# Kernel tuning notes

Hardware: AMD Instinct MI355X
Metric: run time of the kernel (lower is better)

The kernel has to match this reference:

```python
import jax, jax.numpy as jnp
import numpy as np

MUL = 16            # multiplicity of 0e and 1o irreps (in and out)
N_NODES = 10000
N_EDGES = 160000
EDGE_FDIM = 128
H_DIM = 128
WNUM = 4 * MUL * MUL  # 4 instructions x (16 u x 1 v x 16 w) = 1024 weights per edge


def setup_inputs() -> dict:
    key = jax.random.key(0)
    ks = jax.random.split(key, 6)
    x = jax.random.normal(ks[0], (N_NODES, 4 * MUL), dtype=jnp.float32)  # 16x0e + 16x1o -> dim 64
    edge_index = jax.random.randint(ks[1], (2, N_EDGES), 0, N_NODES, dtype=jnp.int32)
    edge_attr = jax.random.normal(ks[2], (N_EDGES, EDGE_FDIM), dtype=jnp.float32)
    edge_sh = jax.random.normal(ks[3], (N_EDGES, 4), dtype=jnp.float32)  # 1x0e + 1x1o
    fc_w1 = jax.random.normal(ks[4], (EDGE_FDIM, H_DIM), dtype=jnp.float32) / np.sqrt(EDGE_FDIM)
    fc_b1 = jnp.zeros((H_DIM,), jnp.float32)
    fc_w2 = jax.random.normal(ks[5], (H_DIM, WNUM), dtype=jnp.float32) / np.sqrt(H_DIM)
    fc_b2 = jnp.zeros((WNUM,), jnp.float32)
    return dict(x=x, edge_index=edge_index, edge_attr=edge_attr, edge_sh=edge_sh,
                fc_w1=fc_w1, fc_b1=fc_b1, fc_w2=fc_w2, fc_b2=fc_b2)


def _tensor_product(xe, edge_sh, w):
    """FullyConnectedTensorProduct('16x0e+16x1o', '1x0e+1x1o', '16x0e+16x1o'),
    shared_weights=False. Instructions (uvw, v=1):
      0e x 0e -> 0e ; 0e x 1o -> 1o ; 1o x 0e -> 1o ; 1o x 1o -> 0e (dot / sqrt(3)).
    Path alpha = 1/sqrt(fan_in) with fan_in = 2*MUL per output irrep (2 paths x 16x1)."""
    x0 = xe[:, :MUL]                          # [E, 16] scalars
    x1 = xe[:, MUL:].reshape(-1, MUL, 3)      # [E, 16, 3] vectors
    sh0 = edge_sh[:, 0:1]                     # [E, 1]
    sh1 = edge_sh[:, 1:4]                     # [E, 3]
    wp = w.reshape(-1, 4, MUL, MUL)           # [E, 4 paths, u, w]
    w00, w01, w10, w11 = wp[:, 0], wp[:, 1], wp[:, 2], wp[:, 3]
    alpha = 1.0 / np.sqrt(2.0 * MUL)
    dot = jnp.einsum('eum,em->eu', x1, sh1)   # 1o . 1o -> 0e
    out0 = alpha * (jnp.einsum('eu,euw->ew', x0 * sh0, w00)
                    + jnp.einsum('eu,euw->ew', dot, w11) / np.sqrt(3.0))  # [E, 16]
    out1 = alpha * (jnp.einsum('eu,euw,em->ewm', x0, w01, sh1)
                    + jnp.einsum('eum,euw->ewm', x1 * sh0[:, :, None], w10))  # [E, 16, 3]
    return jnp.concatenate([out0, out1.reshape(-1, 3 * MUL)], axis=-1)  # [E, 64]


def reference(x, edge_index, edge_attr, edge_sh, fc_w1, fc_b1, fc_w2, fc_b2):
    src, dst = edge_index[0], edge_index[1]
    # per-edge tensor-product weights from edge features (dropout p=0 -> identity)
    w = jax.nn.relu(edge_attr @ fc_w1 + fc_b1) @ fc_w2 + fc_b2       # [E, 1024]
    tp_out = _tensor_product(x[src], edge_sh, w)                      # gather + TP
    seg = jax.ops.segment_sum(tp_out, dst, num_segments=N_NODES)      # scatter-add
    cnt = jax.ops.segment_sum(jnp.ones((N_EDGES,), tp_out.dtype), dst, num_segments=N_NODES)
    out = seg / jnp.maximum(cnt, 1.0)[:, None]                        # mean aggregation
    # residual: out_dim == in_dim (64), so F.pad is a no-op
    return out + x
```

## Files before the change

### kernel.cpp

```cpp
#include <hip/hip_runtime.h>
#include <stdint.h>

#define E_TOTAL 160000
#define NODES   10000
#define FDIM    128
#define HDIM    128
#define WN      1024
#define CDIM    64
#define EPB     32
#define NTHR    256

typedef __bf16 bf16x8 __attribute__((ext_vector_type(8)));
typedef __bf16 bf16x4 __attribute__((ext_vector_type(4)));
typedef float  f32x4  __attribute__((ext_vector_type(4)));

#define MFMA16(a,b,c) __builtin_amdgcn_mfma_f32_16x16x32_bf16(a,b,c,0,0,0)

#define WS_W1B (512*1024)
#define WS_CNT (576*1024)

__device__ __forceinline__ f32x4 ntload4(const float* p) {
    return __builtin_nontemporal_load((const f32x4*)p);
}

__global__ void prep_kernel(const float* __restrict__ W1, const float* __restrict__ W2,
                            __bf16* __restrict__ W1B, __bf16* __restrict__ W2B,
                            float* __restrict__ out_acc, int* __restrict__ cnt) {
    const int b   = blockIdx.x;
    const int tid = threadIdx.x;
    if (b < 72) {
        const float* W = (b < 64) ? W2 : W1;
        __bf16* outB   = (b < 64) ? W2B : W1B;
        const int N    = (b < 64) ? WN : HDIM;
        const int tile = (b < 64) ? b : (b - 64);
        const int lane = tid & 63, ks = tid >> 6;
        const int n  = tile * 16 + (lane & 15);
        const int k0 = ks * 32 + (lane >> 4) * 8;
        bf16x8 hi;
        #pragma unroll
        for (int j = 0; j < 8; ++j) hi[j] = (__bf16)W[(size_t)(k0 + j) * N + n];
        *(bf16x8*)(outB + ((size_t)(tile * 4 + ks) * 64 + lane) * 8) = hi;
    } else {
        const int zt     = (b - 72) * NTHR + tid;
        const int stride = ((int)gridDim.x - 72) * NTHR;
        const float4 z4 = make_float4(0.f, 0.f, 0.f, 0.f);
        for (int i = zt; i < NODES * CDIM / 4; i += stride) ((float4*)out_acc)[i] = z4;
        for (int i = zt; i < NODES; i += stride) cnt[i] = 0;
    }
}

#define ZS 68
__global__ __launch_bounds__(NTHR, 4)
void fused_edge_kernel(const float* __restrict__ x,
                       const int*   __restrict__ edge_index,
                       const float* __restrict__ edge_attr,
                       const float* __restrict__ edge_sh,
                       const float* __restrict__ fc_b1,
                       const float* __restrict__ fc_b2,
                       const __bf16* __restrict__ W1B,
                       const __bf16* __restrict__ W2B,
                       float* __restrict__ out_acc,
                       int*   __restrict__ cnt)
{
    __shared__ __align__(16) char s_arena[25152];
    __bf16* s_attr = (__bf16*)s_arena;
    __bf16* s_h    = (__bf16*)s_arena;
    float (*s_f)[16][32] = (float (*)[16][32])(s_arena + 8192);
    float*  s_b2s  = (float*)(s_arena + 20480);
    float (*s_sh1)[36] = (float (*)[36])(s_arena + 24576);
    int*    s_dst  = (int*)(s_arena + 25024);

    const int tid  = threadIdx.x;
    const int w    = tid >> 6;
    const int th   = w >> 1;
    const int kh   = w & 1;
    const int lane = tid & 63;
    const int quad = lane >> 4;
    const int li   = lane & 15;
    const int e0   = blockIdx.x * EPB;

    if (lane < 32) {
        const int e  = lane;
        const int up = w * 4;
        const int ge = e0 + e;
        const int src = edge_index[ge];
        const f32x4 sh4 = ntload4(edge_sh + (size_t)ge * 4);
        if (tid < EPB) {
            const int d = edge_index[E_TOTAL + ge];
            s_dst[e] = d;
            atomicAdd(&cnt[d], 1);
            s_sh1[0][e] = sh4.y; s_sh1[1][e] = sh4.z; s_sh1[2][e] = sh4.w;
        }
        const float* xp = x + (size_t)src * CDIM;
        const float4 x0v = *(const float4*)(xp + up);
        const float4 xa  = *(const float4*)(xp + 16 + up * 3);
        const float4 xb  = *(const float4*)(xp + 16 + up * 3 + 4);
        const float4 xc  = *(const float4*)(xp + 16 + up * 3 + 8);
        const float x1v[4][3] = {
            {xa.x, xa.y, xa.z}, {xa.w, xb.x, xb.y},
            {xb.z, xb.w, xc.x}, {xc.y, xc.z, xc.w}};
        const float x0a[4] = {x0v.x, x0v.y, x0v.z, x0v.w};
        const float alpha = 0.17677669529663689f;
        const float ai3   = alpha * 0.57735026918962576f;
        const float sh0 = sh4.x;
        #pragma unroll
        for (int j = 0; j < 4; ++j) {
            const int u = up + j;
            const float x0u = x0a[j];
            s_f[0][u][e] = alpha * sh0 * x0u;
            s_f[1][u][e] = alpha * x0u;
            s_f[2][u][e] = alpha * sh0 * x1v[j][0];
            s_f[3][u][e] = alpha * sh0 * x1v[j][1];
            s_f[4][u][e] = alpha * sh0 * x1v[j][2];
            s_f[5][u][e] = ai3 * (x1v[j][0]*sh4.y + x1v[j][1]*sh4.z + x1v[j][2]*sh4.w);
        }
    }
    #pragma unroll
    for (int t4 = 0; t4 < 4; ++t4) {
        const int t = tid + t4 * NTHR;
        const int e = t >> 5, i4 = t & 31;
        const f32x4 v = ntload4(edge_attr + (size_t)(e0 + e) * FDIM + i4 * 4);
        const int f = i4 >> 3, j0 = (i4 & 1) * 4, qc = (i4 >> 1) & 3;
        const int g = e >> 4, lc = e & 15;
        bf16x4 bv = {(__bf16)v[0], (__bf16)v[1], (__bf16)v[2], (__bf16)v[3]};
        *(bf16x4*)(s_attr + (((f * 2 + g) * 64 + qc * 16 + lc) * 8 + j0)) = bv;
    }
    *(f32x4*)&s_b2s[tid * 4] = *(const f32x4*)(fc_b2 + tid * 4);
    __syncthreads();

    {
        const int nt0 = w * 2;
        const float b1a = fc_b1[nt0 * 16 + li];
        const float b1b = fc_b1[(nt0 + 1) * 16 + li];
        bf16x8 A1[2][4];
        #pragma unroll
        for (int g = 0; g < 2; ++g)
            #pragma unroll
            for (int ks = 0; ks < 4; ++ks)
                A1[g][ks] = *(const bf16x8*)(s_attr + ((ks * 2 + g) * 64 + lane) * 8);
        __syncthreads();
        #pragma unroll
        for (int nt2 = 0; nt2 < 2; ++nt2) {
            const int nt = nt0 + nt2;
            const float bias = nt2 ? b1b : b1a;
            bf16x8 Bf[4];
            #pragma unroll
            for (int ks = 0; ks < 4; ++ks)
                Bf[ks] = *(const bf16x8*)(W1B + ((size_t)(nt * 4 + ks) * 64 + lane) * 8);
            f32x4 acc[2];
            #pragma unroll
            for (int g = 0; g < 2; ++g) acc[g] = (f32x4){bias, bias, bias, bias};
            #pragma unroll
            for (int ks = 0; ks < 4; ++ks)
                #pragma unroll
                for (int g = 0; g < 2; ++g) acc[g] = MFMA16(A1[g][ks], Bf[ks], acc[g]);
            const int f  = nt >> 1;
            const int qc = (2 * (nt & 1) + (li >> 3)) & 3;
            const int j  = li & 7;
            #pragma unroll
            for (int g = 0; g < 2; ++g)
                #pragma unroll
                for (int r = 0; r < 4; ++r)
                    s_h[((f * 2 + g) * 64 + qc * 16 + (quad * 4 + r)) * 8 + j] =
                        (__bf16)fmaxf(acc[g][r], 0.f);
        }
    }
    __syncthreads();

    bf16x8 A2[2][2];
    #pragma unroll
    for (int g = 0; g < 2; ++g)
        #pragma unroll
        for (int k2 = 0; k2 < 2; ++k2)
            A2[g][k2] = *(const bf16x8*)(s_h + (((kh * 2 + k2) * 2 + g) * 64 + lane) * 8);

    f32x4 o0[2];
    f32x4 o1[2][3];
    #pragma unroll
    for (int g = 0; g < 2; ++g) {
        o0[g] = (f32x4){0.f, 0.f, 0.f, 0.f};
        #pragma unroll
        for (int m = 0; m < 3; ++m) o1[g][m] = (f32x4){0.f, 0.f, 0.f, 0.f};
    }
    const int tbase = th * 32;
    const __bf16* Wp = W2B + ((size_t)(tbase * 4 + kh * 2) * 64 + lane) * 8;
    bf16x8 P[2][2];
    #pragma unroll
    for (int s = 0; s < 2; ++s)
        #pragma unroll
        for (int k2 = 0; k2 < 2; ++k2)
            P[s][k2] = *(const bf16x8*)(Wp + (s * 4 + k2) * 512);

    #pragma unroll
    for (int half = 0; half < 2; ++half) {
        #pragma unroll
        for (int cc = 0; cc < 16; ++cc) {
            const int c = half * 16 + cc;
            const int u = cc;
            const bf16x8 b0 = P[c & 1][0];
            const bf16x8 b1 = P[c & 1][1];
            if (c + 2 < 32) {
                #pragma unroll
                for (int k2 = 0; k2 < 2; ++k2)
                    P[c & 1][k2] = *(const bf16x8*)(Wp + ((c + 2) * 4 + k2) * 512);
            }
            f32x4 acc[2];
            if (kh == 0) {
                const float b2v = s_b2s[(tbase + c) * 16 + li];
                acc[0] = (f32x4){b2v, b2v, b2v, b2v};
                acc[1] = acc[0];
            } else {
                acc[0] = (f32x4){0.f, 0.f, 0.f, 0.f};
                acc[1] = acc[0];
            }
            #pragma unroll
            for (int g = 0; g < 2; ++g) {
                acc[g] = MFMA16(A2[g][0], b0, acc[g]);
                acc[g] = MFMA16(A2[g][1], b1, acc[g]);
            }
            if (th == 0) {
                if (half == 0) {
                    #pragma unroll
                    for (int g = 0; g < 2; ++g)
                        o0[g] += *(const f32x4*)&s_f[0][u][g * 16 + quad * 4] * acc[g];
                } else {
                    #pragma unroll
                    for (int g = 0; g < 2; ++g)
                        o1[g][0] += *(const f32x4*)&s_f[1][u][g * 16 + quad * 4] * acc[g];
                }
            } else {
                if (half == 0) {
                    #pragma unroll
                    for (int g = 0; g < 2; ++g)
                        #pragma unroll
                        for (int m = 0; m < 3; ++m)
                            o1[g][m] += *(const f32x4*)&s_f[2 + m][u][g * 16 + quad * 4] * acc[g];
                } else {
                    #pragma unroll
                    for (int g = 0; g < 2; ++g)
                        o0[g] += *(const f32x4*)&s_f[5][u][g * 16 + quad * 4] * acc[g];
                }
            }
        }
    }
    if (th == 0) {
        #pragma unroll
        for (int g = 0; g < 2; ++g) {
            const f32x4 t1 = o1[g][0];
            o1[g][2] = t1 * *(const f32x4*)&s_sh1[2][g * 16 + quad * 4];
            o1[g][1] = t1 * *(const f32x4*)&s_sh1[1][g * 16 + quad * 4];
            o1[g][0] = t1 * *(const f32x4*)&s_sh1[0][g * 16 + quad * 4];
        }
    }

    float* zA = (float*)s_arena;
    float* zB = (float*)(s_arena + 8704);
    __syncthreads();
    {
        float* zm = (th == 0) ? zA : zB;
        if (kh == 1) {
            #pragma unroll
            for (int g = 0; g < 2; ++g)
                #pragma unroll
                for (int r = 0; r < 4; ++r) {
                    float* row = zm + (g * 16 + quad * 4 + r) * ZS;
                    row[li] = o0[g][r];
                    #pragma unroll
                    for (int m = 0; m < 3; ++m) row[16 + li * 3 + m] = o1[g][m][r];
                }
        }
        __syncthreads();
        if (kh == 0) {
            #pragma unroll
            for (int g = 0; g < 2; ++g)
                #pragma unroll
                for (int r = 0; r < 4; ++r) {
                    float* row = zm + (g * 16 + quad * 4 + r) * ZS;
                    row[li] += o0[g][r];
                    #pragma unroll
                    for (int m = 0; m < 3; ++m) row[16 + li * 3 + m] += o1[g][m][r];
                }
        }
    }
    __syncthreads();
    {
        const int ebase = w * 8;
        #pragma unroll
        for (int i = 0; i < 8; ++i) {
            const int e = ebase + i;
            const float v = zA[e * ZS + lane] + zB[e * ZS + lane];
            unsafeAtomicAdd(out_acc + (size_t)s_dst[e] * CDIM + lane, v);
        }
    }
}

__global__ void finalize_kernel(const float* __restrict__ x,
                                const int*   __restrict__ cnt,
                                float*       __restrict__ out)
{
    const int idx = blockIdx.x * blockDim.x + threadIdx.x;
    if (idx < NODES * CDIM) {
        const int n = idx >> 6;
        const float c = (float)(cnt[n] > 1 ? cnt[n] : 1);
        out[idx] = out[idx] / c + x[idx];
    }
}

extern "C" void kernel_launch(void* const* d_in, const int* in_sizes, int n_in,
                              void* d_out, int out_size, void* d_ws, size_t ws_size,
                              hipStream_t stream) {
    (void)in_sizes; (void)n_in; (void)out_size; (void)ws_size;
    const float* x          = (const float*)d_in[0];
    const int*   edge_index = (const int*)  d_in[1];
    const float* edge_attr  = (const float*)d_in[2];
    const float* edge_sh    = (const float*)d_in[3];
    const float* fc_w1      = (const float*)d_in[4];
    const float* fc_b1      = (const float*)d_in[5];
    const float* fc_w2      = (const float*)d_in[6];
    const float* fc_b2      = (const float*)d_in[7];
    float*  out = (float*)d_out;
    __bf16* W2B = (__bf16*)d_ws;
    __bf16* W1B = (__bf16*)((char*)d_ws + WS_W1B);
    int*    cnt = (int*)((char*)d_ws + WS_CNT);

    prep_kernel<<<256, NTHR, 0, stream>>>(fc_w1, fc_w2, W1B, W2B, out, cnt);
    fused_edge_kernel<<<E_TOTAL / EPB, NTHR, 0, stream>>>(
        x, edge_index, edge_attr, edge_sh, fc_b1, fc_b2, W1B, W2B, out, cnt);
    finalize_kernel<<<(NODES * CDIM + NTHR - 1) / NTHR, NTHR, 0, stream>>>(x, cnt, out);
}
```

Baseline: 222.6 us.

## Process 64 edges per block with 512 threads to share W2 loads

Doubles the edges per block from 32 to 64 and the threads from 256 to 512, splitting waves into two edge halves that each run the existing per-edge MFMA pipeline. The aim is to halve the number of blocks and the per-block global traffic for W1/W2/bias weight fragments relative to the edges processed. In exchange it raises shared memory to about 46KB per block and changes launch bounds to 6, which may limit occupancy or force register pressure.

```diff
diff --git a/kernel.cpp b/kernel.cpp
--- a/kernel.cpp
+++ b/kernel.cpp
@@ -7,8 +7,8 @@
 #define HDIM    128
 #define WN      1024
 #define CDIM    64
-#define EPB     32
-#define NTHR    256
+#define EPB     64
+#define NTHR    512
 
 typedef __bf16 bf16x8 __attribute__((ext_vector_type(8)));
 typedef __bf16 bf16x4 __attribute__((ext_vector_type(4)));
@@ -33,24 +33,28 @@
         __bf16* outB   = (b < 64) ? W2B : W1B;
         const int N    = (b < 64) ? WN : HDIM;
         const int tile = (b < 64) ? b : (b - 64);
-        const int lane = tid & 63, ks = tid >> 6;
-        const int n  = tile * 16 + (lane & 15);
-        const int k0 = ks * 32 + (lane >> 4) * 8;
-        bf16x8 hi;
-        #pragma unroll
-        for (int j = 0; j < 8; ++j) hi[j] = (__bf16)W[(size_t)(k0 + j) * N + n];
-        *(bf16x8*)(outB + ((size_t)(tile * 4 + ks) * 64 + lane) * 8) = hi;
+        const int lane = tid & 63, ks = (tid >> 6) & 3;
+        if (tid < 256) {
+            const int n  = tile * 16 + (lane & 15);
+            const int k0 = ks * 32 + (lane >> 4) * 8;
+            bf16x8 hi;
+            #pragma unroll
+            for (int j = 0; j < 8; ++j) hi[j] = (__bf16)W[(size_t)(k0 + j) * N + n];
+            *(bf16x8*)(outB + ((size_t)(tile * 4 + ks) * 64 + lane) * 8) = hi;
+        }
     } else {
-        const int zt     = (b - 72) * NTHR + tid;
-        const int stride = ((int)gridDim.x - 72) * NTHR;
-        const float4 z4 = make_float4(0.f, 0.f, 0.f, 0.f);
-        for (int i = zt; i < NODES * CDIM / 4; i += stride) ((float4*)out_acc)[i] = z4;
-        for (int i = zt; i < NODES; i += stride) cnt[i] = 0;
+        const int zt     = (b - 72) * 256 + (tid & 255);
+        const int stride = ((int)gridDim.x - 72) * 256;
+        if (tid < 256) {
+            const float4 z4 = make_float4(0.f, 0.f, 0.f, 0.f);
+            for (int i = zt; i < NODES * CDIM / 4; i += stride) ((float4*)out_acc)[i] = z4;
+            for (int i = zt; i < NODES; i += stride) cnt[i] = 0;
+        }
     }
 }
 
 #define ZS 68
-__global__ __launch_bounds__(NTHR, 4)
+__global__ __launch_bounds__(NTHR, 6)
 void fused_edge_kernel(const float* __restrict__ x,
                        const int*   __restrict__ edge_index,
                        const float* __restrict__ edge_attr,
@@ -62,30 +66,33 @@
                        float* __restrict__ out_acc,
                        int*   __restrict__ cnt)
 {
-    __shared__ __align__(16) char s_arena[25152];
+    __shared__ __align__(16) char s_arena[46128];
     __bf16* s_attr = (__bf16*)s_arena;
     __bf16* s_h    = (__bf16*)s_arena;
-    float (*s_f)[16][32] = (float (*)[16][32])(s_arena + 8192);
-    float*  s_b2s  = (float*)(s_arena + 20480);
-    float (*s_sh1)[36] = (float (*)[36])(s_arena + 24576);
-    int*    s_dst  = (int*)(s_arena + 25024);
+    float (*s_f)[16][64] = (float (*)[16][64])(s_arena + 16384);
+    float*  s_b2s  = (float*)(s_arena + 40960);
+    float (*s_sh1)[68] = (float (*)[68])(s_arena + 45056);
+    int*    s_dst  = (int*)(s_arena + 45872);
 
     const int tid  = threadIdx.x;
     const int w    = tid >> 6;
-    const int th   = w >> 1;
+    const int eh   = w >> 2;
+    const int th   = (w >> 1) & 1;
     const int kh   = w & 1;
+    const int uq   = w & 3;
     const int lane = tid & 63;
     const int quad = lane >> 4;
     const int li   = lane & 15;
     const int e0   = blockIdx.x * EPB;
+    const int eoff = eh * 32;
 
     if (lane < 32) {
-        const int e  = lane;
-        const int up = w * 4;
+        const int e  = eoff + lane;
+        const int up = uq * 4;
         const int ge = e0 + e;
         const int src = edge_index[ge];
         const f32x4 sh4 = ntload4(edge_sh + (size_t)ge * 4);
-        if (tid < EPB) {
+        if (uq == 0) {
             const int d = edge_index[E_TOTAL + ge];
             s_dst[e] = d;
             atomicAdd(&cnt[d], 1);
@@ -123,64 +130,62 @@
         const int f = i4 >> 3, j0 = (i4 & 1) * 4, qc = (i4 >> 1) & 3;
         const int g = e >> 4, lc = e & 15;
         bf16x4 bv = {(__bf16)v[0], (__bf16)v[1], (__bf16)v[2], (__bf16)v[3]};
-        *(bf16x4*)(s_attr + (((f * 2 + g) * 64 + qc * 16 + lc) * 8 + j0)) = bv;
-    }
-    *(f32x4*)&s_b2s[tid * 4] = *(const f32x4*)(fc_b2 + tid * 4);
+        *(bf16x4*)(s_attr + (((f * 4 + g) * 64 + qc * 16 + lc) * 8 + j0)) = bv;
+    }
+    if (tid < 256) *(f32x4*)&s_b2s[tid * 4] = *(const f32x4*)(fc_b2 + tid * 4);
     __syncthreads();
 
     {
-        const int nt0 = w * 2;
-        const float b1a = fc_b1[nt0 * 16 + li];
-        const float b1b = fc_b1[(nt0 + 1) * 16 + li];
+        const int gbase = eh * 2;
         bf16x8 A1[2][4];
         #pragma unroll
-        for (int g = 0; g < 2; ++g)
+        for (int g2 = 0; g2 < 2; ++g2)
             #pragma unroll
             for (int ks = 0; ks < 4; ++ks)
-                A1[g][ks] = *(const bf16x8*)(s_attr + ((ks * 2 + g) * 64 + lane) * 8);
+                A1[g2][ks] = *(const bf16x8*)(s_attr + (((ks * 4 + gbase + g2) * 64 + lane) * 8));
         __syncthreads();
         #pragma unroll
         for (int nt2 = 0; nt2 < 2; ++nt2) {
-            const int nt = nt0 + nt2;
-            const float bias = nt2 ? b1b : b1a;
+            const int nt = uq * 2 + nt2;
+            const float bias = fc_b1[nt * 16 + li];
             bf16x8 Bf[4];
             #pragma unroll
             for (int ks = 0; ks < 4; ++ks)
                 Bf[ks] = *(const bf16x8*)(W1B + ((size_t)(nt * 4 + ks) * 64 + lane) * 8);
             f32x4 acc[2];
             #pragma unroll
-            for (int g = 0; g < 2; ++g) acc[g] = (f32x4){bias, bias, bias, bias};
+            for (int g2 = 0; g2 < 2; ++g2) acc[g2] = (f32x4){bias, bias, bias, bias};
             #pragma unroll
             for (int ks = 0; ks < 4; ++ks)
                 #pragma unroll
-                for (int g = 0; g < 2; ++g) acc[g] = MFMA16(A1[g][ks], Bf[ks], acc[g]);
-            const int f  = nt >> 1;
+                for (int g2 = 0; g2 < 2; ++g2) acc[g2] = MFMA16(A1[g2][ks], Bf[ks], acc[g2]);
+            const int f  = uq;
             const int qc = (2 * (nt & 1) + (li >> 3)) & 3;
             const int j  = li & 7;
             #pragma unroll
-            for (int g = 0; g < 2; ++g)
+            for (int g2 = 0; g2 < 2; ++g2)
                 #pragma unroll
                 for (int r = 0; r < 4; ++r)
-                    s_h[((f * 2 + g) * 64 + qc * 16 + (quad * 4 + r)) * 8 + j] =
-                        (__bf16)fmaxf(acc[g][r], 0.f);
+                    s_h[((f * 4 + gbase + g2) * 64 + qc * 16 + (quad * 4 + r)) * 8 + j] =
+                        (__bf16)fmaxf(acc[g2][r], 0.f);
         }
     }
     __syncthreads();
 
     bf16x8 A2[2][2];
     #pragma unroll
-    for (int g = 0; g < 2; ++g)
+    for (int g2 = 0; g2 < 2; ++g2)
         #pragma unroll
         for (int k2 = 0; k2 < 2; ++k2)
-            A2[g][k2] = *(const bf16x8*)(s_h + (((kh * 2 + k2) * 2 + g) * 64 + lane) * 8);
+            A2[g2][k2] = *(const bf16x8*)(s_h + (((kh * 2 + k2) * 4 + eh * 2 + g2) * 64 + lane) * 8);
 
     f32x4 o0[2];
     f32x4 o1[2][3];
     #pragma unroll
-    for (int g = 0; g < 2; ++g) {
-        o0[g] = (f32x4){0.f, 0.f, 0.f, 0.f};
-        #pragma unroll
-        for (int m = 0; m < 3; ++m) o1[g][m] = (f32x4){0.f, 0.f, 0.f, 0.f};
+    for (int g2 = 0; g2 < 2; ++g2) {
+        o0[g2] = (f32x4){0.f, 0.f, 0.f, 0.f};
+        #pragma unroll
+        for (int m = 0; m < 3; ++m) o1[g2][m] = (f32x4){0.f, 0.f, 0.f, 0.f};
     }
     const int tbase = th * 32;
     const __bf16* Wp = W2B + ((size_t)(tbase * 4 + kh * 2) * 64 + lane) * 8;
@@ -214,71 +219,71 @@
                 acc[1] = acc[0];
             }
             #pragma unroll
-            for (int g = 0; g < 2; ++g) {
-                acc[g] = MFMA16(A2[g][0], b0, acc[g]);
-                acc[g] = MFMA16(A2[g][1], b1, acc[g]);
+            for (int g2 = 0; g2 < 2; ++g2) {
+                acc[g2] = MFMA16(A2[g2][0], b0, acc[g2]);
+                acc[g2] = MFMA16(A2[g2][1], b1, acc[g2]);
             }
             if (th == 0) {
                 if (half == 0) {
                     #pragma unroll
-                    for (int g = 0; g < 2; ++g)
-                        o0[g] += *(const f32x4*)&s_f[0][u][g * 16 + quad * 4] * acc[g];
+                    for (int g2 = 0; g2 < 2; ++g2)
+                        o0[g2] += *(const f32x4*)&s_f[0][u][eoff + g2 * 16 + quad * 4] * acc[g2];
                 } else {
                     #pragma unroll
-                    for (int g = 0; g < 2; ++g)
-                        o1[g][0] += *(const f32x4*)&s_f[1][u][g * 16 + quad * 4] * acc[g];
+                    for (int g2 = 0; g2 < 2; ++g2)
+                        o1[g2][0] += *(const f32x4*)&s_f[1][u][eoff + g2 * 16 + quad * 4] * acc[g2];
                 }
             } else {
                 if (half == 0) {
                     #pragma unroll
-                    for (int g = 0; g < 2; ++g)
+                    for (int g2 = 0; g2 < 2; ++g2)
                         #pragma unroll
                         for (int m = 0; m < 3; ++m)
-                            o1[g][m] += *(const f32x4*)&s_f[2 + m][u][g * 16 + quad * 4] * acc[g];
+                            o1[g2][m] += *(const f32x4*)&s_f[2 + m][u][eoff + g2 * 16 + quad * 4] * acc[g2];
                 } else {
                     #pragma unroll
-                    for (int g = 0; g < 2; ++g)
-                        o0[g] += *(const f32x4*)&s_f[5][u][g * 16 + quad * 4] * acc[g];
+                    for (int g2 = 0; g2 < 2; ++g2)
+                        o0[g2] += *(const f32x4*)&s_f[5][u][eoff + g2 * 16 + quad * 4] * acc[g2];
                 }
             }
         }
     }
     if (th == 0) {
         #pragma unroll
-        for (int g = 0; g < 2; ++g) {
-            const f32x4 t1 = o1[g][0];
-            o1[g][2] = t1 * *(const f32x4*)&s_sh1[2][g * 16 + quad * 4];
-            o1[g][1] = t1 * *(const f32x4*)&s_sh1[1][g * 16 + quad * 4];
-            o1[g][0] = t1 * *(const f32x4*)&s_sh1[0][g * 16 + quad * 4];
+        for (int g2 = 0; g2 < 2; ++g2) {
+            const f32x4 t1 = o1[g2][0];
+            o1[g2][2] = t1 * *(const f32x4*)&s_sh1[2][eoff + g2 * 16 + quad * 4];
+            o1[g2][1] = t1 * *(const f32x4*)&s_sh1[1][eoff + g2 * 16 + quad * 4];
+            o1[g2][0] = t1 * *(const f32x4*)&s_sh1[0][eoff + g2 * 16 + quad * 4];
         }
     }
 
     float* zA = (float*)s_arena;
-    float* zB = (float*)(s_arena + 8704);
+    float* zB = (float*)(s_arena + 17408);
     __syncthreads();
     {
         float* zm = (th == 0) ? zA : zB;
         if (kh == 1) {
             #pragma unroll
-            for (int g = 0; g < 2; ++g)
+            for (int g2 = 0; g2 < 2; ++g2)
                 #pragma unroll
                 for (int r = 0; r < 4; ++r) {
-                    float* row = zm + (g * 16 + quad * 4 + r) * ZS;
-                    row[li] = o0[g][r];
-                    #pragma unroll
-                    for (int m = 0; m < 3; ++m) row[16 + li * 3 + m] = o1[g][m][r];
+                    float* row = zm + (eoff + g2 * 16 + quad * 4 + r) * ZS;
+                    row[li] = o0[g2][r];
+                    #pragma unroll
+                    for (int m = 0; m < 3; ++m) row[16 + li * 3 + m] = o1[g2][m][r];
                 }
         }
         __syncthreads();
         if (kh == 0) {
             #pragma unroll
-            for (int g = 0; g < 2; ++g)
+            for (int g2 = 0; g2 < 2; ++g2)
                 #pragma unroll
                 for (int r = 0; r < 4; ++r) {
-                    float* row = zm + (g * 16 + quad * 4 + r) * ZS;
-                    row[li] += o0[g][r];
-                    #pragma unroll
-                    for (int m = 0; m < 3; ++m) row[16 + li * 3 + m] += o1[g][m][r];
+                    float* row = zm + (eoff + g2 * 16 + quad * 4 + r) * ZS;
+                    row[li] += o0[g2][r];
+                    #pragma unroll
+                    for (int m = 0; m < 3; ++m) row[16 + li * 3 + m] += o1[g2][m][r];
                 }
         }
     }
@@ -323,8 +328,8 @@
     __bf16* W1B = (__bf16*)((char*)d_ws + WS_W1B);
     int*    cnt = (int*)((char*)d_ws + WS_CNT);
 
-    prep_kernel<<<256, NTHR, 0, stream>>>(fc_w1, fc_w2, W1B, W2B, out, cnt);
+    prep_kernel<<<256, 256, 0, stream>>>(fc_w1, fc_w2, W1B, W2B, out, cnt);
     fused_edge_kernel<<<E_TOTAL / EPB, NTHR, 0, stream>>>(
         x, edge_index, edge_attr, edge_sh, fc_b1, fc_b2, W1B, W2B, out, cnt);
-    finalize_kernel<<<(NODES * CDIM + NTHR - 1) / NTHR, NTHR, 0, stream>>>(x, cnt, out);
-}
+    finalize_kernel<<<(NODES * CDIM + 255) / 256, 256, 0, stream>>>(x, cnt, out);
+}
```

Measured after the change: 421.3 us. 1.89x slower.

## Make edge kernel persistent over 5 groups with register prefetch of next group

Applied to the files above, without the earlier changes.

The edge kernel now launches 1000 blocks, and each block loops over 5 groups of 32 edges instead of handling one group per block. While the current group's MLP and tensor-product MFMAs run, the next group's indices, spherical harmonics, edge attributes and gathered node features are loaded into registers. The goal is to hide global-memory latency and amortise block launch and bias loading. In exchange it adds register pressure and an extra barrier per iteration, and with fewer blocks each CU may hold fewer waves.

```diff
diff --git a/kernel.cpp b/kernel.cpp
--- a/kernel.cpp
+++ b/kernel.cpp
@@ -9,6 +9,8 @@
 #define CDIM    64
 #define EPB     32
 #define NTHR    256
+#define GPB     5
+#define NBLK    1000
 
 typedef __bf16 bf16x8 __attribute__((ext_vector_type(8)));
 typedef __bf16 bf16x4 __attribute__((ext_vector_type(4)));
@@ -77,219 +79,269 @@
     const int lane = tid & 63;
     const int quad = lane >> 4;
     const int li   = lane & 15;
-    const int e0   = blockIdx.x * EPB;
-
-    if (lane < 32) {
-        const int e  = lane;
-        const int up = w * 4;
-        const int ge = e0 + e;
-        const int src = edge_index[ge];
-        const f32x4 sh4 = ntload4(edge_sh + (size_t)ge * 4);
-        if (tid < EPB) {
-            const int d = edge_index[E_TOTAL + ge];
-            s_dst[e] = d;
-            atomicAdd(&cnt[d], 1);
-            s_sh1[0][e] = sh4.y; s_sh1[1][e] = sh4.z; s_sh1[2][e] = sh4.w;
-        }
-        const float* xp = x + (size_t)src * CDIM;
-        const float4 x0v = *(const float4*)(xp + up);
-        const float4 xa  = *(const float4*)(xp + 16 + up * 3);
-        const float4 xb  = *(const float4*)(xp + 16 + up * 3 + 4);
-        const float4 xc  = *(const float4*)(xp + 16 + up * 3 + 8);
-        const float x1v[4][3] = {
-            {xa.x, xa.y, xa.z}, {xa.w, xb.x, xb.y},
-            {xb.z, xb.w, xc.x}, {xc.y, xc.z, xc.w}};
-        const float x0a[4] = {x0v.x, x0v.y, x0v.z, x0v.w};
-        const float alpha = 0.17677669529663689f;
-        const float ai3   = alpha * 0.57735026918962576f;
-        const float sh0 = sh4.x;
-        #pragma unroll
-        for (int j = 0; j < 4; ++j) {
-            const int u = up + j;
-            const float x0u = x0a[j];
-            s_f[0][u][e] = alpha * sh0 * x0u;
-            s_f[1][u][e] = alpha * x0u;
-            s_f[2][u][e] = alpha * sh0 * x1v[j][0];
-            s_f[3][u][e] = alpha * sh0 * x1v[j][1];
-            s_f[4][u][e] = alpha * sh0 * x1v[j][2];
-            s_f[5][u][e] = ai3 * (x1v[j][0]*sh4.y + x1v[j][1]*sh4.z + x1v[j][2]*sh4.w);
-        }
-    }
-    #pragma unroll
-    for (int t4 = 0; t4 < 4; ++t4) {
-        const int t = tid + t4 * NTHR;
-        const int e = t >> 5, i4 = t & 31;
-        const f32x4 v = ntload4(edge_attr + (size_t)(e0 + e) * FDIM + i4 * 4);
-        const int f = i4 >> 3, j0 = (i4 & 1) * 4, qc = (i4 >> 1) & 3;
-        const int g = e >> 4, lc = e & 15;
-        bf16x4 bv = {(__bf16)v[0], (__bf16)v[1], (__bf16)v[2], (__bf16)v[3]};
-        *(bf16x4*)(s_attr + (((f * 2 + g) * 64 + qc * 16 + lc) * 8 + j0)) = bv;
-    }
+    const int gbase = blockIdx.x * GPB;
+
     *(f32x4*)&s_b2s[tid * 4] = *(const f32x4*)(fc_b2 + tid * 4);
-    __syncthreads();
-
-    {
-        const int nt0 = w * 2;
-        const float b1a = fc_b1[nt0 * 16 + li];
-        const float b1b = fc_b1[(nt0 + 1) * 16 + li];
-        bf16x8 A1[2][4];
-        #pragma unroll
-        for (int g = 0; g < 2; ++g)
-            #pragma unroll
-            for (int ks = 0; ks < 4; ++ks)
-                A1[g][ks] = *(const bf16x8*)(s_attr + ((ks * 2 + g) * 64 + lane) * 8);
-        __syncthreads();
-        #pragma unroll
-        for (int nt2 = 0; nt2 < 2; ++nt2) {
-            const int nt = nt0 + nt2;
-            const float bias = nt2 ? b1b : b1a;
-            bf16x8 Bf[4];
-            #pragma unroll
-            for (int ks = 0; ks < 4; ++ks)
-                Bf[ks] = *(const bf16x8*)(W1B + ((size_t)(nt * 4 + ks) * 64 + lane) * 8);
-            f32x4 acc[2];
-            #pragma unroll
-            for (int g = 0; g < 2; ++g) acc[g] = (f32x4){bias, bias, bias, bias};
-            #pragma unroll
-            for (int ks = 0; ks < 4; ++ks)
-                #pragma unroll
-                for (int g = 0; g < 2; ++g) acc[g] = MFMA16(A1[g][ks], Bf[ks], acc[g]);
-            const int f  = nt >> 1;
-            const int qc = (2 * (nt & 1) + (li >> 3)) & 3;
-            const int j  = li & 7;
-            #pragma unroll
-            for (int g = 0; g < 2; ++g)
-                #pragma unroll
-                for (int r = 0; r < 4; ++r)
-                    s_h[((f * 2 + g) * 64 + qc * 16 + (quad * 4 + r)) * 8 + j] =
-                        (__bf16)fmaxf(acc[g][r], 0.f);
-        }
-    }
-    __syncthreads();
-
-    bf16x8 A2[2][2];
-    #pragma unroll
-    for (int g = 0; g < 2; ++g)
-        #pragma unroll
-        for (int k2 = 0; k2 < 2; ++k2)
-            A2[g][k2] = *(const bf16x8*)(s_h + (((kh * 2 + k2) * 2 + g) * 64 + lane) * 8);
-
-    f32x4 o0[2];
-    f32x4 o1[2][3];
-    #pragma unroll
-    for (int g = 0; g < 2; ++g) {
-        o0[g] = (f32x4){0.f, 0.f, 0.f, 0.f};
-        #pragma unroll
-        for (int m = 0; m < 3; ++m) o1[g][m] = (f32x4){0.f, 0.f, 0.f, 0.f};
-    }
+
     const int tbase = th * 32;
     const __bf16* Wp = W2B + ((size_t)(tbase * 4 + kh * 2) * 64 + lane) * 8;
-    bf16x8 P[2][2];
-    #pragma unroll
-    for (int s = 0; s < 2; ++s)
-        #pragma unroll
-        for (int k2 = 0; k2 < 2; ++k2)
-            P[s][k2] = *(const bf16x8*)(Wp + (s * 4 + k2) * 512);
-
-    #pragma unroll
-    for (int half = 0; half < 2; ++half) {
-        #pragma unroll
-        for (int cc = 0; cc < 16; ++cc) {
-            const int c = half * 16 + cc;
-            const int u = cc;
-            const bf16x8 b0 = P[c & 1][0];
-            const bf16x8 b1 = P[c & 1][1];
-            if (c + 2 < 32) {
-                #pragma unroll
-                for (int k2 = 0; k2 < 2; ++k2)
-                    P[c & 1][k2] = *(const bf16x8*)(Wp + ((c + 2) * 4 + k2) * 512);
-            }
-            f32x4 acc[2];
+
+    f32x4 avp[4]; f32x4 shp = {0.f, 0.f, 0.f, 0.f};
+    float4 xvp[4]; int srcp = 0, dstp = 0;
+    {
+        const int e0n = gbase * EPB;
+        if (lane < 32) {
+            const int ge = e0n + lane;
+            srcp = edge_index[ge];
+            if (w == 0) dstp = edge_index[E_TOTAL + ge];
+            shp = ntload4(edge_sh + (size_t)ge * 4);
+        }
+        #pragma unroll
+        for (int t4 = 0; t4 < 4; ++t4) {
+            const int t = tid + t4 * NTHR;
+            const int e = t >> 5, i4 = t & 31;
+            avp[t4] = ntload4(edge_attr + (size_t)(e0n + e) * FDIM + i4 * 4);
+        }
+        if (lane < 32) {
+            const float* xp = x + (size_t)srcp * CDIM;
+            const int up = w * 4;
+            xvp[0] = *(const float4*)(xp + up);
+            xvp[1] = *(const float4*)(xp + 16 + up * 3);
+            xvp[2] = *(const float4*)(xp + 16 + up * 3 + 4);
+            xvp[3] = *(const float4*)(xp + 16 + up * 3 + 8);
+        }
+    }
+
+    for (int j = 0; j < GPB; ++j) {
+        if (j > 0) __syncthreads();
+
+        if (lane < 32) {
+            const int e  = lane;
+            const int up = w * 4;
+            if (w == 0) {
+                s_dst[e] = dstp;
+                atomicAdd(&cnt[dstp], 1);
+                s_sh1[0][e] = shp.y; s_sh1[1][e] = shp.z; s_sh1[2][e] = shp.w;
+            }
+            const float4 x0v = xvp[0], xa = xvp[1], xb = xvp[2], xc = xvp[3];
+            const float x1v[4][3] = {
+                {xa.x, xa.y, xa.z}, {xa.w, xb.x, xb.y},
+                {xb.z, xb.w, xc.x}, {xc.y, xc.z, xc.w}};
+            const float x0a[4] = {x0v.x, x0v.y, x0v.z, x0v.w};
+            const float alpha = 0.17677669529663689f;
+            const float ai3   = alpha * 0.57735026918962576f;
+            const float sh0 = shp.x;
+            #pragma unroll
+            for (int jj = 0; jj < 4; ++jj) {
+                const int u = up + jj;
+                const float x0u = x0a[jj];
+                s_f[0][u][e] = alpha * sh0 * x0u;
+                s_f[1][u][e] = alpha * x0u;
+                s_f[2][u][e] = alpha * sh0 * x1v[jj][0];
+                s_f[3][u][e] = alpha * sh0 * x1v[jj][1];
+                s_f[4][u][e] = alpha * sh0 * x1v[jj][2];
+                s_f[5][u][e] = ai3 * (x1v[jj][0]*shp.y + x1v[jj][1]*shp.z + x1v[jj][2]*shp.w);
+            }
+        }
+        #pragma unroll
+        for (int t4 = 0; t4 < 4; ++t4) {
+            const int t = tid + t4 * NTHR;
+            const int e = t >> 5, i4 = t & 31;
+            const f32x4 v = avp[t4];
+            const int f = i4 >> 3, j0 = (i4 & 1) * 4, qc = (i4 >> 1) & 3;
+            const int g = e >> 4, lc = e & 15;
+            bf16x4 bv = {(__bf16)v[0], (__bf16)v[1], (__bf16)v[2], (__bf16)v[3]};
+            *(bf16x4*)(s_attr + (((f * 2 + g) * 64 + qc * 16 + lc) * 8 + j0)) = bv;
+        }
+        __syncthreads();
+
+        const bool pf  = (j + 1 < GPB);
+        const int  e0n = (gbase + j + 1) * EPB;
+        if (pf && lane < 32) {
+            const int ge = e0n + lane;
+            srcp = edge_index[ge];
+            if (w == 0) dstp = edge_index[E_TOTAL + ge];
+            shp = ntload4(edge_sh + (size_t)ge * 4);
+        }
+
+        {
+            const int nt0 = w * 2;
+            const float b1a = fc_b1[nt0 * 16 + li];
+            const float b1b = fc_b1[(nt0 + 1) * 16 + li];
+            bf16x8 A1[2][4];
+            #pragma unroll
+            for (int g = 0; g < 2; ++g)
+                #pragma unroll
+                for (int ks = 0; ks < 4; ++ks)
+                    A1[g][ks] = *(const bf16x8*)(s_attr + ((ks * 2 + g) * 64 + lane) * 8);
+            __syncthreads();
+            #pragma unroll
+            for (int nt2 = 0; nt2 < 2; ++nt2) {
+                const int nt = nt0 + nt2;
+                const float bias = nt2 ? b1b : b1a;
+                bf16x8 Bf[4];
+                #pragma unroll
+                for (int ks = 0; ks < 4; ++ks)
+                    Bf[ks] = *(const bf16x8*)(W1B + ((size_t)(nt * 4 + ks) * 64 + lane) * 8);
+                f32x4 acc[2];
+                #pragma unroll
+                for (int g = 0; g < 2; ++g) acc[g] = (f32x4){bias, bias, bias, bias};
+                #pragma unroll
+                for (int ks = 0; ks < 4; ++ks)
+                    #pragma unroll
+                    for (int g = 0; g < 2; ++g) acc[g] = MFMA16(A1[g][ks], Bf[ks], acc[g]);
+                const int f  = nt >> 1;
+                const int qc = (2 * (nt & 1) + (li >> 3)) & 3;
+                const int jb = li & 7;
+                #pragma unroll
+                for (int g = 0; g < 2; ++g)
+                    #pragma unroll
+                    for (int r = 0; r < 4; ++r)
+                        s_h[((f * 2 + g) * 64 + qc * 16 + (quad * 4 + r)) * 8 + jb] =
+                            (__bf16)fmaxf(acc[g][r], 0.f);
+            }
+        }
+        __syncthreads();
+
+        bf16x8 A2[2][2];
+        #pragma unroll
+        for (int g = 0; g < 2; ++g)
+            #pragma unroll
+            for (int k2 = 0; k2 < 2; ++k2)
+                A2[g][k2] = *(const bf16x8*)(s_h + (((kh * 2 + k2) * 2 + g) * 64 + lane) * 8);
+
+        f32x4 o0[2];
+        f32x4 o1[2][3];
+        #pragma unroll
+        for (int g = 0; g < 2; ++g) {
+            o0[g] = (f32x4){0.f, 0.f, 0.f, 0.f};
+            #pragma unroll
+            for (int m = 0; m < 3; ++m) o1[g][m] = (f32x4){0.f, 0.f, 0.f, 0.f};
+        }
+        bf16x8 P[2][2];
+        #pragma unroll
+        for (int s = 0; s < 2; ++s)
+            #pragma unroll
+            for (int k2 = 0; k2 < 2; ++k2)
+                P[s][k2] = *(const bf16x8*)(Wp + (s * 4 + k2) * 512);
+
+        #pragma unroll
+        for (int half = 0; half < 2; ++half) {
+            #pragma unroll
+            for (int cc = 0; cc < 16; ++cc) {
+                const int c = half * 16 + cc;
+                const int u = cc;
+                const bf16x8 b0 = P[c & 1][0];
+                const bf16x8 b1 = P[c & 1][1];
+                if (c + 2 < 32) {
+                    #pragma unroll
+                    for (int k2 = 0; k2 < 2; ++k2)
+                        P[c & 1][k2] = *(const bf16x8*)(Wp + ((c + 2) * 4 + k2) * 512);
+                }
+                f32x4 acc[2];
+                if (kh == 0) {
+                    const float b2v = s_b2s[(tbase + c) * 16 + li];
+                    acc[0] = (f32x4){b2v, b2v, b2v, b2v};
+                    acc[1] = acc[0];
+                } else {
+                    acc[0] = (f32x4){0.f, 0.f, 0.f, 0.f};
+                    acc[1] = acc[0];
+                }
+                #pragma unroll
+                for (int g = 0; g < 2; ++g) {
+                    acc[g] = MFMA16(A2[g][0], b0, acc[g]);
+                    acc[g] = MFMA16(A2[g][1], b1, acc[g]);
+                }
+                if (th == 0) {
+                    if (half == 0) {
+                        #pragma unroll
+                        for (int g = 0; g < 2; ++g)
+                            o0[g] += *(const f32x4*)&s_f[0][u][g * 16 + quad * 4] * acc[g];
+                    } else {
+                        #pragma unroll
+                        for (int g = 0; g < 2; ++g)
+                            o1[g][0] += *(const f32x4*)&s_f[1][u][g * 16 + quad * 4] * acc[g];
+                    }
+                } else {
+                    if (half == 0) {
+                        #pragma unroll
+                        for (int g = 0; g < 2; ++g)
+                            #pragma unroll
+                            for (int m = 0; m < 3; ++m)
+                                o1[g][m] += *(const f32x4*)&s_f[2 + m][u][g * 16 + quad * 4] * acc[g];
+                    } else {
+                        #pragma unroll
+                        for (int g = 0; g < 2; ++g)
+                            o0[g] += *(const f32x4*)&s_f[5][u][g * 16 + quad * 4] * acc[g];
+                    }
+                }
+            }
+        }
+        if (th == 0) {
+            #pragma unroll
+            for (int g = 0; g < 2; ++g) {
+                const f32x4 t1 = o1[g][0];
+                o1[g][2] = t1 * *(const f32x4*)&s_sh1[2][g * 16 + quad * 4];
+                o1[g][1] = t1 * *(const f32x4*)&s_sh1[1][g * 16 + quad * 4];
+                o1[g][0] = t1 * *(const f32x4*)&s_sh1[0][g * 16 + quad * 4];
+            }
+        }
+
+        if (pf) {
+            #pragma unroll
+            for (int t4 = 0; t4 < 4; ++t4) {
+                const int t = tid + t4 * NTHR;
+                const int e = t >> 5, i4 = t & 31;
+                avp[t4] = ntload4(edge_attr + (size_t)(e0n + e) * FDIM + i4 * 4);
+            }
+            if (lane < 32) {
+                const float* xp = x + (size_t)srcp * CDIM;
+                const int up = w * 4;
+                xvp[0] = *(const float4*)(xp + up);
+                xvp[1] = *(const float4*)(xp + 16 + up * 3);
+                xvp[2] = *(const float4*)(xp + 16 + up * 3 + 4);
+                xvp[3] = *(const float4*)(xp + 16 + up * 3 + 8);
+            }
+        }
+
+        float* zA = (float*)s_arena;
+        float* zB = (float*)(s_arena + 8704);
+        __syncthreads();
+        {
+            float* zm = (th == 0) ? zA : zB;
+            if (kh == 1) {
+                #pragma unroll
+                for (int g = 0; g < 2; ++g)
+                    #pragma unroll
+                    for (int r = 0; r < 4; ++r) {
+                        float* row = zm + (g * 16 + quad * 4 + r) * ZS;
+                        row[li] = o0[g][r];
+                        #pragma unroll
+                        for (int m = 0; m < 3; ++m) row[16 + li * 3 + m] = o1[g][m][r];
+                    }
+            }
+            __syncthreads();
             if (kh == 0) {
-                const float b2v = s_b2s[(tbase + c) * 16 + li];
-                acc[0] = (f32x4){b2v, b2v, b2v, b2v};
-                acc[1] = acc[0];
-            } else {
-                acc[0] = (f32x4){0.f, 0.f, 0.f, 0.f};
-                acc[1] = acc[0];
-            }
-            #pragma unroll
-            for (int g = 0; g < 2; ++g) {
-                acc[g] = MFMA16(A2[g][0], b0, acc[g]);
-                acc[g] = MFMA16(A2[g][1], b1, acc[g]);
-            }
-            if (th == 0) {
-                if (half == 0) {
-                    #pragma unroll
-                    for (int g = 0; g < 2; ++g)
-                        o0[g] += *(const f32x4*)&s_f[0][u][g * 16 + quad * 4] * acc[g];
-                } else {
-                    #pragma unroll
-                    for (int g = 0; g < 2; ++g)
-                        o1[g][0] += *(const f32x4*)&s_f[1][u][g * 16 + quad * 4] * acc[g];
-                }
-            } else {
-                if (half == 0) {
-                    #pragma unroll
-                    for (int g = 0; g < 2; ++g)
-                        #pragma unroll
-                        for (int m = 0; m < 3; ++m)
-                            o1[g][m] += *(const f32x4*)&s_f[2 + m][u][g * 16 + quad * 4] * acc[g];
-                } else {
-                    #pragma unroll
-                    for (int g = 0; g < 2; ++g)
-                        o0[g] += *(const f32x4*)&s_f[5][u][g * 16 + quad * 4] * acc[g];
-                }
-            }
-        }
-    }
-    if (th == 0) {
-        #pragma unroll
-        for (int g = 0; g < 2; ++g) {
-            const f32x4 t1 = o1[g][0];
-            o1[g][2] = t1 * *(const f32x4*)&s_sh1[2][g * 16 + quad * 4];
-            o1[g][1] = t1 * *(const f32x4*)&s_sh1[1][g * 16 + quad * 4];
-            o1[g][0] = t1 * *(const f32x4*)&s_sh1[0][g * 16 + quad * 4];
-        }
-    }
-
-    float* zA = (float*)s_arena;
-    float* zB = (float*)(s_arena + 8704);
-    __syncthreads();
-    {
-        float* zm = (th == 0) ? zA : zB;
-        if (kh == 1) {
-            #pragma unroll
-            for (int g = 0; g < 2; ++g)
-                #pragma unroll
-                for (int r = 0; r < 4; ++r) {
-                    float* row = zm + (g * 16 + quad * 4 + r) * ZS;
-                    row[li] = o0[g][r];
-                    #pragma unroll
-                    for (int m = 0; m < 3; ++m) row[16 + li * 3 + m] = o1[g][m][r];
-                }
+                #pragma unroll
+                for (int g = 0; g < 2; ++g)
+                    #pragma unroll
+                    for (int r = 0; r < 4; ++r) {
+                        float* row = zm + (g * 16 + quad * 4 + r) * ZS;
+                        row[li] += o0[g][r];
+                        #pragma unroll
+                        for (int m = 0; m < 3; ++m) row[16 + li * 3 + m] += o1[g][m][r];
+                    }
+            }
         }
         __syncthreads();
-        if (kh == 0) {
-            #pragma unroll
-            for (int g = 0; g < 2; ++g)
-                #pragma unroll
-                for (int r = 0; r < 4; ++r) {
-                    float* row = zm + (g * 16 + quad * 4 + r) * ZS;
-                    row[li] += o0[g][r];
-                    #pragma unroll
-                    for (int m = 0; m < 3; ++m) row[16 + li * 3 + m] += o1[g][m][r];
-                }
-        }
-    }
-    __syncthreads();
-    {
-        const int ebase = w * 8;
-        #pragma unroll
-        for (int i = 0; i < 8; ++i) {
-            const int e = ebase + i;
-            const float v = zA[e * ZS + lane] + zB[e * ZS + lane];
-            unsafeAtomicAdd(out_acc + (size_t)s_dst[e] * CDIM + lane, v);
+        {
+            const int ebase = w * 8;
+            #pragma unroll
+            for (int i = 0; i < 8; ++i) {
+                const int e = ebase + i;
+                const float v = zA[e * ZS + lane] + zB[e * ZS + lane];
+                unsafeAtomicAdd(out_acc + (size_t)s_dst[e] * CDIM + lane, v);
+            }
         }
     }
 }
@@ -324,7 +376,7 @@
     int*    cnt = (int*)((char*)d_ws + WS_CNT);
 
     prep_kernel<<<256, NTHR, 0, stream>>>(fc_w1, fc_w2, W1B, W2B, out, cnt);
-    fused_edge_kernel<<<E_TOTAL / EPB, NTHR, 0, stream>>>(
+    fused_edge_kernel<<<NBLK, NTHR, 0, stream>>>(
         x, edge_index, edge_attr, edge_sh, fc_b1, fc_b2, W1B, W2B, out, cnt);
     finalize_kernel<<<(NODES * CDIM + NTHR - 1) / NTHR, NTHR, 0, stream>>>(x, cnt, out);
 }
```

After: 565.5 us. +154.0%, slower.

## Process 64 edges per block to amortize W2 weight loads over more MFMAs

Applied to the files above, without the earlier changes.

Doubles the edges handled per block from 32 to 64. The first-layer MLP work is re-split across waves by edge group and N-half, and every per-edge accumulator array grows from 2 to 4 MFMA row groups. Each W2 fragment loaded from global memory now feeds twice as many MFMAs, which halves total W2 traffic. In exchange, register and LDS use roughly double (arena about 46KB, launch bounds lowered to 3 blocks/SM), so occupancy drops and the grid has half as many blocks.

```diff
diff --git a/kernel.cpp b/kernel.cpp
--- a/kernel.cpp
+++ b/kernel.cpp
@@ -7,7 +7,7 @@
 #define HDIM    128
 #define WN      1024
 #define CDIM    64
-#define EPB     32
+#define EPB     64
 #define NTHR    256
 
 typedef __bf16 bf16x8 __attribute__((ext_vector_type(8)));
@@ -50,7 +50,7 @@
 }
 
 #define ZS 68
-__global__ __launch_bounds__(NTHR, 4)
+__global__ __launch_bounds__(NTHR, 3)
 void fused_edge_kernel(const float* __restrict__ x,
                        const int*   __restrict__ edge_index,
                        const float* __restrict__ edge_attr,
@@ -62,13 +62,13 @@
                        float* __restrict__ out_acc,
                        int*   __restrict__ cnt)
 {
-    __shared__ __align__(16) char s_arena[25152];
+    __shared__ __align__(16) char s_arena[46128];
     __bf16* s_attr = (__bf16*)s_arena;
     __bf16* s_h    = (__bf16*)s_arena;
-    float (*s_f)[16][32] = (float (*)[16][32])(s_arena + 8192);
-    float*  s_b2s  = (float*)(s_arena + 20480);
-    float (*s_sh1)[36] = (float (*)[36])(s_arena + 24576);
-    int*    s_dst  = (int*)(s_arena + 25024);
+    float (*s_f)[16][64] = (float (*)[16][64])(s_arena + 16384);
+    float*  s_b2s  = (float*)(s_arena + 40960);
+    float (*s_sh1)[68] = (float (*)[68])(s_arena + 45056);
+    int*    s_dst  = (int*)(s_arena + 45872);
 
     const int tid  = threadIdx.x;
     const int w    = tid >> 6;
@@ -79,13 +79,13 @@
     const int li   = lane & 15;
     const int e0   = blockIdx.x * EPB;
 
-    if (lane < 32) {
+    {
         const int e  = lane;
         const int up = w * 4;
         const int ge = e0 + e;
         const int src = edge_index[ge];
         const f32x4 sh4 = ntload4(edge_sh + (size_t)ge * 4);
-        if (tid < EPB) {
+        if (w == 0) {
             const int d = edge_index[E_TOTAL + ge];
             s_dst[e] = d;
             atomicAdd(&cnt[d], 1);
@@ -116,68 +116,67 @@
         }
     }
     #pragma unroll
-    for (int t4 = 0; t4 < 4; ++t4) {
+    for (int t4 = 0; t4 < 8; ++t4) {
         const int t = tid + t4 * NTHR;
         const int e = t >> 5, i4 = t & 31;
         const f32x4 v = ntload4(edge_attr + (size_t)(e0 + e) * FDIM + i4 * 4);
         const int f = i4 >> 3, j0 = (i4 & 1) * 4, qc = (i4 >> 1) & 3;
         const int g = e >> 4, lc = e & 15;
         bf16x4 bv = {(__bf16)v[0], (__bf16)v[1], (__bf16)v[2], (__bf16)v[3]};
-        *(bf16x4*)(s_attr + (((f * 2 + g) * 64 + qc * 16 + lc) * 8 + j0)) = bv;
+        *(bf16x4*)(s_attr + (((f * 4 + g) * 64 + qc * 16 + lc) * 8 + j0)) = bv;
     }
     *(f32x4*)&s_b2s[tid * 4] = *(const f32x4*)(fc_b2 + tid * 4);
     __syncthreads();
 
     {
-        const int nt0 = w * 2;
-        const float b1a = fc_b1[nt0 * 16 + li];
-        const float b1b = fc_b1[(nt0 + 1) * 16 + li];
+        const int gp = w >> 1;
+        const int nh = w & 1;
         bf16x8 A1[2][4];
         #pragma unroll
-        for (int g = 0; g < 2; ++g)
+        for (int g2 = 0; g2 < 2; ++g2)
             #pragma unroll
             for (int ks = 0; ks < 4; ++ks)
-                A1[g][ks] = *(const bf16x8*)(s_attr + ((ks * 2 + g) * 64 + lane) * 8);
+                A1[g2][ks] = *(const bf16x8*)(s_attr + (((ks * 4 + gp * 2 + g2) * 64 + lane) * 8));
         __syncthreads();
         #pragma unroll
-        for (int nt2 = 0; nt2 < 2; ++nt2) {
-            const int nt = nt0 + nt2;
-            const float bias = nt2 ? b1b : b1a;
+        for (int nt2 = 0; nt2 < 4; ++nt2) {
+            const int nt = nh * 4 + nt2;
+            const float bias = fc_b1[nt * 16 + li];
             bf16x8 Bf[4];
             #pragma unroll
             for (int ks = 0; ks < 4; ++ks)
                 Bf[ks] = *(const bf16x8*)(W1B + ((size_t)(nt * 4 + ks) * 64 + lane) * 8);
             f32x4 acc[2];
             #pragma unroll
-            for (int g = 0; g < 2; ++g) acc[g] = (f32x4){bias, bias, bias, bias};
+            for (int g2 = 0; g2 < 2; ++g2) acc[g2] = (f32x4){bias, bias, bias, bias};
             #pragma unroll
             for (int ks = 0; ks < 4; ++ks)
                 #pragma unroll
-                for (int g = 0; g < 2; ++g) acc[g] = MFMA16(A1[g][ks], Bf[ks], acc[g]);
+                for (int g2 = 0; g2 < 2; ++g2) acc[g2] = MFMA16(A1[g2][ks], Bf[ks], acc[g2]);
             const int f  = nt >> 1;
             const int qc = (2 * (nt & 1) + (li >> 3)) & 3;
-            const int j  = li & 7;
-            #pragma unroll
-            for (int g = 0; g < 2; ++g)
+            const int jb = li & 7;
+            #pragma unroll
+            for (int g2 = 0; g2 < 2; ++g2)
                 #pragma unroll
                 for (int r = 0; r < 4; ++r)
-                    s_h[((f * 2 + g) * 64 + qc * 16 + (quad * 4 + r)) * 8 + j] =
-                        (__bf16)fmaxf(acc[g][r], 0.f);
+                    s_h[((f * 4 + gp * 2 + g2) * 64 + qc * 16 + (quad * 4 + r)) * 8 + jb] =
+                        (__bf16)fmaxf(acc[g2][r], 0.f);
         }
     }
     __syncthreads();
 
-    bf16x8 A2[2][2];
-    #pragma unroll
-    for (int g = 0; g < 2; ++g)
+    bf16x8 A2[4][2];
+    #pragma unroll
+    for (int g = 0; g < 4; ++g)
         #pragma unroll
         for (int k2 = 0; k2 < 2; ++k2)
-            A2[g][k2] = *(const bf16x8*)(s_h + (((kh * 2 + k2) * 2 + g) * 64 + lane) * 8);
-
-    f32x4 o0[2];
-    f32x4 o1[2][3];
-    #pragma unroll
-    for (int g = 0; g < 2; ++g) {
+            A2[g][k2] = *(const bf16x8*)(s_h + (((kh * 2 + k2) * 4 + g) * 64 + lane) * 8);
+
+    f32x4 o0[4];
+    f32x4 o1[4][3];
+    #pragma unroll
+    for (int g = 0; g < 4; ++g) {
         o0[g] = (f32x4){0.f, 0.f, 0.f, 0.f};
         #pragma unroll
         for (int m = 0; m < 3; ++m) o1[g][m] = (f32x4){0.f, 0.f, 0.f, 0.f};
@@ -204,40 +203,40 @@
                 for (int k2 = 0; k2 < 2; ++k2)
                     P[c & 1][k2] = *(const bf16x8*)(Wp + ((c + 2) * 4 + k2) * 512);
             }
-            f32x4 acc[2];
+            f32x4 acc[4];
             if (kh == 0) {
                 const float b2v = s_b2s[(tbase + c) * 16 + li];
-                acc[0] = (f32x4){b2v, b2v, b2v, b2v};
-                acc[1] = acc[0];
+                #pragma unroll
+                for (int g = 0; g < 4; ++g) acc[g] = (f32x4){b2v, b2v, b2v, b2v};
             } else {
-                acc[0] = (f32x4){0.f, 0.f, 0.f, 0.f};
-                acc[1] = acc[0];
+                #pragma unroll
+                for (int g = 0; g < 4; ++g) acc[g] = (f32x4){0.f, 0.f, 0.f, 0.f};
             }
             #pragma unroll
-            for (int g = 0; g < 2; ++g) {
+            for (int g = 0; g < 4; ++g) {
                 acc[g] = MFMA16(A2[g][0], b0, acc[g]);
                 acc[g] = MFMA16(A2[g][1], b1, acc[g]);
             }
             if (th == 0) {
                 if (half == 0) {
                     #pragma unroll
-                    for (int g = 0; g < 2; ++g)
+                    for (int g = 0; g < 4; ++g)
                         o0[g] += *(const f32x4*)&s_f[0][u][g * 16 + quad * 4] * acc[g];
                 } else {
                     #pragma unroll
-                    for (int g = 0; g < 2; ++g)
+                    for (int g = 0; g < 4; ++g)
                         o1[g][0] += *(const f32x4*)&s_f[1][u][g * 16 + quad * 4] * acc[g];
                 }
             } else {
                 if (half == 0) {
                     #pragma unroll
-                    for (int g = 0; g < 2; ++g)
+                    for (int g = 0; g < 4; ++g)
                         #pragma unroll
                         for (int m = 0; m < 3; ++m)
                             o1[g][m] += *(const f32x4*)&s_f[2 + m][u][g * 16 + quad * 4] * acc[g];
                 } else {
                     #pragma unroll
-                    for (int g = 0; g < 2; ++g)
+                    for (int g = 0; g < 4; ++g)
                         o0[g] += *(const f32x4*)&s_f[5][u][g * 16 + quad * 4] * acc[g];
                 }
             }
@@ -245,7 +244,7 @@
     }
     if (th == 0) {
         #pragma unroll
-        for (int g = 0; g < 2; ++g) {
+        for (int g = 0; g < 4; ++g) {
             const f32x4 t1 = o1[g][0];
             o1[g][2] = t1 * *(const f32x4*)&s_sh1[2][g * 16 + quad * 4];
             o1[g][1] = t1 * *(const f32x4*)&s_sh1[1][g * 16 + quad * 4];
@@ -254,13 +253,13 @@
     }
 
     float* zA = (float*)s_arena;
-    float* zB = (float*)(s_arena + 8704);
+    float* zB = (float*)(s_arena + 17408);
     __syncthreads();
     {
         float* zm = (th == 0) ? zA : zB;
         if (kh == 1) {
             #pragma unroll
-            for (int g = 0; g < 2; ++g)
+            for (int g = 0; g < 4; ++g)
                 #pragma unroll
                 for (int r = 0; r < 4; ++r) {
                     float* row = zm + (g * 16 + quad * 4 + r) * ZS;
@@ -272,7 +271,7 @@
         __syncthreads();
         if (kh == 0) {
             #pragma unroll
-            for (int g = 0; g < 2; ++g)
+            for (int g = 0; g < 4; ++g)
                 #pragma unroll
                 for (int r = 0; r < 4; ++r) {
                     float* row = zm + (g * 16 + quad * 4 + r) * ZS;
@@ -284,9 +283,9 @@
     }
     __syncthreads();
     {
-        const int ebase = w * 8;
-        #pragma unroll
-        for (int i = 0; i < 8; ++i) {
+        const int ebase = w * 16;
+        #pragma unroll
+        for (int i = 0; i < 16; ++i) {
             const int e = ebase + i;
             const float v = zA[e * ZS + lane] + zB[e * ZS + lane];
             unsafeAtomicAdd(out_acc + (size_t)s_dst[e] * CDIM + lane, v);
```

Result: no change. 224.0 us (+0.6%).
